# Optimization experiments

Hardware: AMD Instinct MI355X
Metric: run time of the kernel (lower is better)

The kernel has to match this reference:

```python
import jax, jax.numpy as jnp
import numpy as np

S, IN, H, D, B, BOT, IMG, TXT = 4, 4096, 2048, 6, 1024, 128, 768, 768


def _gelu(x):
    # torch nn.GELU default = exact erf gelu
    return jax.nn.gelu(x, approximate=False)


def _ln(x, g, b, eps=1e-5):
    mu = jnp.mean(x, axis=-1, keepdims=True)
    var = jnp.mean(jnp.square(x - mu), axis=-1, keepdims=True)
    return g * (x - mu) / jnp.sqrt(var + eps) + b


def setup_inputs() -> dict:
    key = jax.random.key(0)
    ks = jax.random.split(key, 16)
    n = lambda k, shp, s=0.02: jax.random.normal(k, shp, dtype=jnp.float32) * s
    return dict(
        voxels=jax.random.normal(ks[0], (B, IN), dtype=jnp.float32),
        subject_ids=jax.random.randint(ks[1], (B,), 0, S, dtype=jnp.int32),
        # per-subject encoder params, stacked on leading subject axis S
        ad_down_w=n(ks[2], (S, IN, BOT)), ad_down_b=n(ks[3], (S, BOT)),
        ad_up_w=n(ks[4], (S, BOT, IN)), ad_up_b=n(ks[5], (S, IN)),
        enc_w=n(ks[6], (S, IN, H)), enc_b=n(ks[7], (S, H)),
        enc_ln_g=jnp.ones((S, H), jnp.float32), enc_ln_b=jnp.zeros((S, H), jnp.float32),
        # shared ResidualStack params, stacked on leading depth axis D
        bb_w=n(ks[8], (D, H, H)), bb_b=n(ks[9], (D, H)),
        bb_ln_g=jnp.ones((D, H), jnp.float32), bb_ln_b=jnp.zeros((D, H), jnp.float32),
        # heads
        img_w=n(ks[10], (H, IMG)), img_b=n(ks[11], (IMG,)),
        txt_w=n(ks[12], (H, TXT)), txt_b=n(ks[13], (TXT,)),
    )


def _forward(voxels, subject_ids, ad_down_w, ad_down_b, ad_up_w, ad_up_b,
             enc_w, enc_b, enc_ln_g, enc_ln_b, bb_w, bb_b, bb_ln_g, bb_ln_b,
             img_w, img_b, txt_w, txt_b):
    # --- subject-routed encoders (dense dispatch over the small fixed subject set) ---
    def enc_one(dw, db, uw, ub, ew, eb, g, be):
        # BottleneckAdapter: x + up(gelu(down(x)))
        h = voxels + _gelu(voxels @ dw + db) @ uw + ub          # [B, IN]
        # Linear -> LayerNorm -> GELU (Dropout is identity in eval)
        return _gelu(_ln(h @ ew + eb, g, be))                    # [B, H]

    feats_all = jax.vmap(enc_one)(ad_down_w, ad_down_b, ad_up_w, ad_up_b,
                                  enc_w, enc_b, enc_ln_g, enc_ln_b)  # [S, B, H]
    x = feats_all[subject_ids, jnp.arange(voxels.shape[0])]          # [B, H] pick own subject

    # --- shared ResidualStack: x = x + gelu(ln(linear(x))) per block ---
    def step(x, p):
        w, b, g, be = p
        return x + _gelu(_ln(x @ w + b, g, be)), None

    x, _ = jax.lax.scan(step, x, (bb_w, bb_b, bb_ln_g, bb_ln_b))

    return x @ img_w + img_b, x @ txt_w + txt_b  # (image_embedding, text_embedding)


def reference(voxels, subject_ids, ad_down_w, ad_down_b, ad_up_w, ad_up_b,
              enc_w, enc_b, enc_ln_g, enc_ln_b, bb_w, bb_b, bb_ln_g, bb_ln_b,
              img_w, img_b, txt_w, txt_b):
    return _forward(voxels, subject_ids, ad_down_w, ad_down_b, ad_up_w, ad_up_b,
                    enc_w, enc_b, enc_ln_g, enc_ln_b, bb_w, bb_b, bb_ln_g, bb_ln_b,
                    img_w, img_b, txt_w, txt_b)
```

## Files before the change

kernel.cpp:

```cpp
#include <hip/hip_runtime.h>
#include <hip/hip_bf16.h>
#include <stdint.h>

typedef __bf16 bf16x8 __attribute__((ext_vector_type(8)));
typedef float  f32x4  __attribute__((ext_vector_type(4)));

#define DEV __device__ __forceinline__

constexpr int SUBJ  = 4;
constexpr int IN    = 4096;
constexpr int H     = 2048;
constexpr int DEPTH = 6;
constexpr int BATCH = 1024;
constexpr int BOT   = 128;
constexpr int IMG   = 768;
constexpr int TXT   = 768;
constexpr int MP    = 1408;
constexpr int MT    = 11;

DEV float gelu_exact(float x){ return 0.5f*x*(1.0f + erff(x*0.70710678118654752440f)); }

DEV uint32_t pk_bf16(float a, float b){
  __hip_bfloat16 ha = __float2bfloat16(a), hb = __float2bfloat16(b);
  return (uint32_t)*reinterpret_cast<uint16_t*>(&ha)
       | ((uint32_t)*reinterpret_cast<uint16_t*>(&hb) << 16);
}

__global__ void sort_kernel(const int* __restrict__ ids, int* __restrict__ rowmap,
                            int* __restrict__ tileS){
  __shared__ int hist[16][4];
  __shared__ int basew[16][4];
  __shared__ int pstart[5];
  int tid = threadIdx.x;
  if (tid < MP) rowmap[tid] = -1;
  if (tid + 1024 < MP) rowmap[tid + 1024] = -1;
  int w = tid >> 6, lane = tid & 63;
  int my = ids[tid];
  unsigned long long mymask = 0ull;
  #pragma unroll
  for (int s = 0; s < 4; ++s){
    unsigned long long m = __ballot(my == s);
    if (lane == 0) hist[w][s] = (int)__popcll(m);
    if (s == my) mymask = m;
  }
  int myrank = (int)__popcll(mymask & ((1ull << lane) - 1ull));
  __syncthreads();
  if (tid == 0){
    for (int s = 0; s < 4; ++s){
      int run = 0;
      for (int ww = 0; ww < 16; ++ww){ basew[ww][s] = run; run += hist[ww][s]; }
      hist[0][s] = run;
    }
    pstart[0] = 0;
    for (int s = 0; s < 4; ++s) pstart[s+1] = pstart[s] + ((hist[0][s] + 127) & ~127);
  }
  __syncthreads();
  int pos = pstart[my] + basew[w][my] + myrank;
  rowmap[pos] = tid;
  if (tid < MT){
    int row0 = tid << 7, s = -1;
    for (int ss = 0; ss < 4; ++ss) if (row0 >= pstart[ss] && row0 < pstart[ss+1]) s = ss;
    tileS[tid] = s;
  }
}

__global__ void gather_voxels(const float* __restrict__ vox, const int* __restrict__ rowmap,
                              __hip_bfloat16* __restrict__ Vs){
  int r = blockIdx.x, tid = threadIdx.x;
  int orig = rowmap[r];
  #pragma unroll
  for (int i = 0; i < 4; ++i){
    int c = (i*256 + tid) << 2;
    float4 v = {0.f,0.f,0.f,0.f};
    if (orig >= 0) v = *reinterpret_cast<const float4*>(vox + (size_t)orig*IN + c);
    __hip_bfloat16 o[4] = {__float2bfloat16(v.x), __float2bfloat16(v.y),
                           __float2bfloat16(v.z), __float2bfloat16(v.w)};
    *reinterpret_cast<uint2*>(Vs + (size_t)r*IN + c) = *reinterpret_cast<const uint2*>(o);
  }
}

enum { EPI_SPLIT = 0, EPI_RES_BF16 = 1, EPI_HEADS = 3 };

template<int EPI, int TAG>
__global__ __launch_bounds__(256, 2)
void gemm_bf16(const __hip_bfloat16* __restrict__ A, int lda,
               const float* __restrict__ Bw, int ldn, long long wsub,
               const int* __restrict__ tileS, const int* __restrict__ rowmap,
               int nx, int qnt, int ksplit,
               const float* __restrict__ bias, int biassub,
               const float* __restrict__ resid, int ldres,
               float* __restrict__ outf, __hip_bfloat16* __restrict__ outb, int ldo,
               size_t pstride, const float* __restrict__ Bw2)
{
  int b   = blockIdx.x;
  int xcd = b & 7;
  int r0  = b >> 3;
  int mt  = r0 % MT;
  int q   = r0 / MT;
  int kzi = xcd / nx + (q / qnt) * (8 / nx);
  int nt  = (q % qnt) * nx + (xcd % nx);

  int s = tileS[mt];
  if (s < 0) return;
  const __hip_bfloat16* Ab = A + (size_t)mt*128*lda;

  const float* Bb;
  int ntl = nt;
  if constexpr (EPI == EPI_HEADS){
    if (nt < 6){ Bb = Bw  + (size_t)nt*128; }
    else       { Bb = Bw2 + (size_t)(nt-6)*128; }
    ntl = nt;
  } else {
    Bb = Bw + (size_t)s*wsub + (size_t)nt*128;
  }

  int kb = kzi * ksplit;
  int nk = ksplit >> 6;

  __shared__ __hip_bfloat16 sA[2][128*64];
  __shared__ __hip_bfloat16 sB[2][128*64];

  int tid = threadIdx.x;
  int lane = tid & 63;
  int wv = tid >> 6, wr = wv >> 1, wc = wv & 1;

  int kq = tid >> 5;
  int nq = tid & 31;
  int n4 = nq << 2;

  f32x4 acc[4][4];
  #pragma unroll
  for (int i = 0; i < 4; ++i)
    #pragma unroll
    for (int j = 0; j < 4; ++j) acc[i][j] = (f32x4){0.f,0.f,0.f,0.f};

  auto stageA = [&](int buf, int k0){
    #pragma unroll
    for (int i = 0; i < 4; ++i){
      int cell = i*256 + tid;
      int row = cell >> 3, cc = cell & 7;
      int kg = k0 + ((cc ^ (row & 7)) << 3);
      __builtin_amdgcn_global_load_lds(
        (const __attribute__((address_space(1))) void*)(Ab + (size_t)row*lda + kg),
        (__attribute__((address_space(3))) void*)(&sA[buf][cell<<3]), 16, 0, 0);
    }
  };

  auto stageB_load = [&](int k0g, float4* F){
    const float* p = Bb + (size_t)(k0g + (kq<<3))*ldn + n4;
    #pragma unroll
    for (int rr = 0; rr < 8; ++rr)
      F[rr] = *reinterpret_cast<const float4*>(p + (size_t)rr*ldn);
  };
  auto stageB_write = [&](int buf, const float4* F){
    #pragma unroll
    for (int j = 0; j < 4; ++j){
      int n = n4 + j;
      int cell = (kq ^ (n >> 3) ^ n) & 7;
      uint4 d;
      d.x = pk_bf16(((const float*)&F[0])[j], ((const float*)&F[1])[j]);
      d.y = pk_bf16(((const float*)&F[2])[j], ((const float*)&F[3])[j]);
      d.z = pk_bf16(((const float*)&F[4])[j], ((const float*)&F[5])[j]);
      d.w = pk_bf16(((const float*)&F[6])[j], ((const float*)&F[7])[j]);
      *reinterpret_cast<uint4*>(&sB[buf][(n<<6) + (cell<<3)]) = d;
    }
  };

  float4 F[8];
  stageB_load(kb, F);
  stageA(0, kb);
  stageB_write(0, F);
  __syncthreads();

  for (int t = 0; t < nk; ++t){
    if (t+1 < nk){
      stageB_load(kb + ((t+1)<<6), F);
      stageA((t+1)&1, kb + ((t+1)<<6));
    }
    const char* baseA = (const char*)(&sA[t&1][0]);
    const char* baseB = (const char*)(&sB[t&1][0]);
    int rA = (wr<<6) + (lane & 15);
    int rB = (wc<<6) + (lane & 15);
    #pragma unroll
    for (int kk = 0; kk < 2; ++kk){
      int koffA = ((((kk<<5) + ((lane>>4)<<3)) << 1)) ^ ((lane & 7) << 4);
      bf16x8 av[4], bv[4];
      #pragma unroll
      for (int f = 0; f < 4; ++f){
        int rowA = rA + f*16;
        av[f] = *reinterpret_cast<const bf16x8*>(baseA + (size_t)rowA*128 + koffA);
        int rowB = rB + f*16;
        int cellB = (((kk<<2) + (lane>>4)) ^ (rowB >> 3) ^ rowB) & 7;
        bv[f] = *reinterpret_cast<const bf16x8*>(baseB + (size_t)rowB*128 + (cellB<<4));
      }
      #pragma unroll
      for (int i = 0; i < 4; ++i)
        #pragma unroll
        for (int j = 0; j < 4; ++j)
          acc[i][j] = __builtin_amdgcn_mfma_f32_16x16x32_bf16(av[i], bv[j], acc[i][j], 0, 0, 0);
    }
    if (t+1 < nk) stageB_write((t+1)&1, F);
    __syncthreads();
  }

  #pragma unroll
  for (int i = 0; i < 4; ++i){
    int rbase = (mt<<7) + (wr<<6) + (i<<4) + ((lane>>4)<<2);
    #pragma unroll
    for (int j = 0; j < 4; ++j){
      int colp = (wc<<6) + (j<<4) + (lane & 15);
      #pragma unroll
      for (int qq = 0; qq < 4; ++qq){
        int r = rbase + qq;
        float v = acc[i][j][qq];
        if constexpr (EPI == EPI_SPLIT){
          int col = (nt<<7) + colp;
          outf[(size_t)kzi*pstride + (size_t)r*ldo + col] = v;
        } else if constexpr (EPI == EPI_RES_BF16){
          int col = (nt<<7) + colp;
          int orig = rowmap[r];
          if (orig >= 0){
            v += bias[(size_t)s*biassub + col] + resid[(size_t)orig*ldres + col];
            outb[(size_t)r*ldo + col] = __float2bfloat16(v);
          }
        } else {
          int col = (ntl<<7) + colp;
          outf[(size_t)kzi*pstride + (size_t)r*ldo + col] = v;
        }
      }
    }
  }
}

__global__ void t1_epilogue(const float* __restrict__ Tp, const float* __restrict__ db,
                            const int* __restrict__ rowmap, const int* __restrict__ tileS,
                            __hip_bfloat16* __restrict__ T1){
  int idx = blockIdx.x*256 + threadIdx.x;
  int r = idx >> 7, c = idx & 127;
  float v = 0.f;
  if (rowmap[r] >= 0){
    int s = tileS[r >> 7];
    float acc = 0.f;
    #pragma unroll
    for (int p = 0; p < 32; ++p) acc += Tp[(size_t)p*MP*BOT + idx];
    v = gelu_exact(acc + db[s*BOT + c]);
  }
  T1[idx] = __float2bfloat16(v);
}

template<int RES, int NPART>
__global__ void ln_gelu_kernel(const float* __restrict__ Zp, size_t pstride,
                               const float* __restrict__ g,
                               const float* __restrict__ b, int gsub,
                               const float* __restrict__ lb,
                               const int* __restrict__ tileS, const int* __restrict__ rowmap,
                               float* __restrict__ Xf, __hip_bfloat16* __restrict__ Xb){
  int r = blockIdx.x, tid = threadIdx.x;
  size_t rowoff = (size_t)r * H;
  int c0 = tid << 3;
  int orig = rowmap[r];
  if (orig < 0){
    float4 zf = {0.f,0.f,0.f,0.f};
    *reinterpret_cast<float4*>(Xf + rowoff + c0)     = zf;
    *reinterpret_cast<float4*>(Xf + rowoff + c0 + 4) = zf;
    uint4 zu = {0u,0u,0u,0u};
    *reinterpret_cast<uint4*>(Xb + rowoff + c0) = zu;
    return;
  }
  int si = gsub ? tileS[r>>7] : 0;
  const float* gp  = g  + (size_t)si*gsub;
  const float* bp  = b  + (size_t)si*gsub;
  const float* lbp = lb + (size_t)si*gsub;
  float z[8];
  #pragma unroll
  for (int j = 0; j < 8; ++j) z[j] = lbp[c0+j];
  #pragma unroll
  for (int p = 0; p < NPART; ++p){
    float4 v1 = *reinterpret_cast<const float4*>(Zp + p*pstride + rowoff + c0);
    float4 v2 = *reinterpret_cast<const float4*>(Zp + p*pstride + rowoff + c0 + 4);
    z[0]+=v1.x; z[1]+=v1.y; z[2]+=v1.z; z[3]+=v1.w;
    z[4]+=v2.x; z[5]+=v2.y; z[6]+=v2.z; z[7]+=v2.w;
  }
  float s1 = 0.f, s2 = 0.f;
  #pragma unroll
  for (int j = 0; j < 8; ++j){ s1 += z[j]; s2 += z[j]*z[j]; }
  #pragma unroll
  for (int m = 32; m >= 1; m >>= 1){ s1 += __shfl_xor(s1, m); s2 += __shfl_xor(s2, m); }
  __shared__ float red[4][2];
  int wv = tid >> 6, lane = tid & 63;
  if (lane == 0){ red[wv][0] = s1; red[wv][1] = s2; }
  __syncthreads();
  s1 = red[0][0]+red[1][0]+red[2][0]+red[3][0];
  s2 = red[0][1]+red[1][1]+red[2][1]+red[3][1];
  const float invH = 1.f / (float)H;
  float mu  = s1 * invH;
  float var = s2 * invH - mu*mu;
  float rs  = rsqrtf(var + 1e-5f);
  float o[8];
  #pragma unroll
  for (int j = 0; j < 8; ++j){
    float t = (z[j]-mu)*rs*gp[c0+j] + bp[c0+j];
    o[j] = gelu_exact(t);
  }
  if constexpr (RES){
    float4 x1 = *reinterpret_cast<const float4*>(Xf + rowoff + c0);
    float4 x2 = *reinterpret_cast<const float4*>(Xf + rowoff + c0 + 4);
    o[0]+=x1.x; o[1]+=x1.y; o[2]+=x1.z; o[3]+=x1.w;
    o[4]+=x2.x; o[5]+=x2.y; o[6]+=x2.z; o[7]+=x2.w;
  }
  float4 w1 = {o[0],o[1],o[2],o[3]}, w2 = {o[4],o[5],o[6],o[7]};
  *reinterpret_cast<float4*>(Xf + rowoff + c0)     = w1;
  *reinterpret_cast<float4*>(Xf + rowoff + c0 + 4) = w2;
  __hip_bfloat16 ob[8];
  #pragma unroll
  for (int j = 0; j < 8; ++j) ob[j] = __float2bfloat16(o[j]);
  *reinterpret_cast<uint4*>(Xb + rowoff + c0) = *reinterpret_cast<const uint4*>(ob);
}

__global__ void head_combine(const float* __restrict__ Hp, size_t pstride,
                             const float* __restrict__ img_b, const float* __restrict__ txt_b,
                             const int* __restrict__ rowmap,
                             float* __restrict__ oimg, float* __restrict__ otxt){
  int r = blockIdx.x;
  int orig = rowmap[r];
  if (orig < 0) return;
  int col = threadIdx.x << 2;
  size_t base = (size_t)r*(IMG+TXT) + col;
  float4 v0 = *reinterpret_cast<const float4*>(Hp + base);
  float4 v1 = *reinterpret_cast<const float4*>(Hp + pstride + base);
  float4 bb = (col < IMG)
            ? *reinterpret_cast<const float4*>(img_b + col)
            : *reinterpret_cast<const float4*>(txt_b + (col - IMG));
  float4 o = {v0.x+v1.x+bb.x, v0.y+v1.y+bb.y, v0.z+v1.z+bb.z, v0.w+v1.w+bb.w};
  if (col < IMG) *reinterpret_cast<float4*>(oimg + (size_t)orig*IMG + col) = o;
  else           *reinterpret_cast<float4*>(otxt + (size_t)orig*TXT + (col-IMG)) = o;
}

extern "C" void kernel_launch(void* const* d_in, const int* in_sizes, int n_in,
                              void* d_out, int out_size, void* d_ws, size_t ws_size,
                              hipStream_t stream){
  (void)in_sizes; (void)n_in; (void)out_size; (void)ws_size;
  const float* vox       = (const float*)d_in[0];
  const int*   ids       = (const int*)  d_in[1];
  const float* ad_down_w = (const float*)d_in[2];
  const float* ad_down_b = (const float*)d_in[3];
  const float* ad_up_w   = (const float*)d_in[4];
  const float* ad_up_b   = (const float*)d_in[5];
  const float* enc_w     = (const float*)d_in[6];
  const float* enc_b     = (const float*)d_in[7];
  const float* enc_ln_g  = (const float*)d_in[8];
  const float* enc_ln_bb = (const float*)d_in[9];
  const float* bb_w      = (const float*)d_in[10];
  const float* bb_b      = (const float*)d_in[11];
  const float* bb_ln_g   = (const float*)d_in[12];
  const float* bb_ln_b   = (const float*)d_in[13];
  const float* img_w     = (const float*)d_in[14];
  const float* img_b     = (const float*)d_in[15];
  const float* txt_w     = (const float*)d_in[16];
  const float* txt_b     = (const float*)d_in[17];
  float* out = (float*)d_out;

  char* wp = (char*)d_ws;
  auto alloc = [&](size_t bytes)->char*{ char* p = wp; wp += (bytes + 255) & ~(size_t)255; return p; };
  int* rowmap = (int*)alloc(MP * sizeof(int));
  int* tileS  = (int*)alloc(MT * sizeof(int));
  __hip_bfloat16* Vs    = (__hip_bfloat16*)alloc((size_t)MP*IN*2);
  float* T1p            = (float*)alloc((size_t)32*MP*BOT*4);
  __hip_bfloat16* T1    = (__hip_bfloat16*)alloc((size_t)MP*BOT*2);
  __hip_bfloat16* Hs    = (__hip_bfloat16*)alloc((size_t)MP*IN*2);
  float* Zp             = (float*)alloc((size_t)8*MP*H*4);
  float* Hp             = (float*)alloc((size_t)2*MP*(IMG+TXT)*4);
  float* Xf             = (float*)alloc((size_t)MP*H*4);
  __hip_bfloat16* Xb    = (__hip_bfloat16*)alloc((size_t)MP*H*2);

  const size_t ZPS = (size_t)MP*H;
  const size_t TPS = (size_t)MP*BOT;
  const size_t HPS = (size_t)MP*(IMG+TXT);

  sort_kernel<<<1, 1024, 0, stream>>>(ids, rowmap, tileS);
  gather_voxels<<<MP, 256, 0, stream>>>(vox, rowmap, Vs);

  gemm_bf16<EPI_SPLIT,1><<<MT*32, 256, 0, stream>>>(
      Vs, IN, ad_down_w, BOT, (long long)IN*BOT, tileS, rowmap, 1, 1, 128,
      nullptr, 0, nullptr, 0, T1p, nullptr, BOT, TPS, nullptr);
  t1_epilogue<<<MP*BOT/256, 256, 0, stream>>>(T1p, ad_down_b, rowmap, tileS, T1);

  gemm_bf16<EPI_RES_BF16,2><<<MT*32, 256, 0, stream>>>(
      T1, BOT, ad_up_w, IN, (long long)BOT*IN, tileS, rowmap, 8, 4, 128,
      ad_up_b, IN, vox, IN, nullptr, Hs, IN, 0, nullptr);

  gemm_bf16<EPI_SPLIT,3><<<MT*16*8, 256, 0, stream>>>(
      Hs, IN, enc_w, H, (long long)IN*H, tileS, rowmap, 1, 16, 512,
      nullptr, 0, nullptr, 0, Zp, nullptr, H, ZPS, nullptr);
  ln_gelu_kernel<0,8><<<MP, 256, 0, stream>>>(Zp, ZPS, enc_ln_g, enc_ln_bb, H, enc_b,
                                              tileS, rowmap, Xf, Xb);

  for (int d = 0; d < DEPTH; ++d){
    gemm_bf16<EPI_SPLIT,4><<<MT*16*2, 256, 0, stream>>>(
        Xb, H, bb_w + (size_t)d*H*H, H, 0, tileS, rowmap, 4, 4, 1024,
        nullptr, 0, nullptr, 0, Zp, nullptr, H, ZPS, nullptr);
    ln_gelu_kernel<1,2><<<MP, 256, 0, stream>>>(Zp, ZPS, bb_ln_g + (size_t)d*H,
                                                bb_ln_b + (size_t)d*H, 0, bb_b + (size_t)d*H,
                                                tileS, rowmap, Xf, Xb);
  }

  gemm_bf16<EPI_HEADS,5><<<MT*12*2, 256, 0, stream>>>(
      Xb, H, img_w, IMG, 0, tileS, rowmap, 4, 3, 1024,
      nullptr, 0, nullptr, 0, Hp, nullptr, IMG+TXT, HPS, txt_w);
  head_combine<<<MP, 384, 0, stream>>>(Hp, HPS, img_b, txt_b, rowmap,
                                       out, out + (size_t)BATCH*IMG);
}
```

Baseline: 496.0 us.

## Pre-convert all weights to bf16 once per call and retune GEMM split-K

Adds a grid-stride kernel that converts every fp32 weight tensor into one contiguous bf16 workspace before the GEMMs. Each GEMM then loads bf16 weights directly, which halves the bytes it streams per K-step and removes the per-tile fp32-to-bf16 packing. It also retunes split-K factors for the down-projection and encoder GEMMs and shrinks the partial-sum buffers to match. The trade-off is a full extra read and write of every weight tensor on each call, about 400 MB of traffic.

```diff
diff --git a/kernel.cpp b/kernel.cpp
--- a/kernel.cpp
+++ b/kernel.cpp
@@ -20,10 +20,28 @@
 
 DEV float gelu_exact(float x){ return 0.5f*x*(1.0f + erff(x*0.70710678118654752440f)); }
 
-DEV uint32_t pk_bf16(float a, float b){
-  __hip_bfloat16 ha = __float2bfloat16(a), hb = __float2bfloat16(b);
-  return (uint32_t)*reinterpret_cast<uint16_t*>(&ha)
-       | ((uint32_t)*reinterpret_cast<uint16_t*>(&hb) << 16);
+DEV uint16_t bf16_bits(float x){
+  __hip_bfloat16 h = __float2bfloat16(x);
+  return *reinterpret_cast<uint16_t*>(&h);
+}
+
+struct CvtSeg { const float* src; size_t dst_off; };
+struct CvtParams { CvtSeg s[6]; size_t total_items; };
+
+__global__ void convert_weights(CvtParams p, __hip_bfloat16* __restrict__ dst){
+  size_t stride = (size_t)gridDim.x * blockDim.x;
+  for (size_t it = (size_t)blockIdx.x*blockDim.x + threadIdx.x; it < p.total_items; it += stride){
+    size_t e = it << 3;
+    int si = 0;
+    #pragma unroll
+    for (int i = 1; i < 6; ++i) if (e >= p.s[i].dst_off) si = i;
+    const float* s = p.s[si].src + (e - p.s[si].dst_off);
+    float4 a = *reinterpret_cast<const float4*>(s);
+    float4 b = *reinterpret_cast<const float4*>(s + 4);
+    uint16_t o[8] = {bf16_bits(a.x), bf16_bits(a.y), bf16_bits(a.z), bf16_bits(a.w),
+                     bf16_bits(b.x), bf16_bits(b.y), bf16_bits(b.z), bf16_bits(b.w)};
+    *reinterpret_cast<uint4*>(dst + e) = *reinterpret_cast<const uint4*>(o);
+  }
 }
 
 __global__ void sort_kernel(const int* __restrict__ ids, int* __restrict__ rowmap,
@@ -84,13 +102,13 @@
 template<int EPI, int TAG>
 __global__ __launch_bounds__(256, 2)
 void gemm_bf16(const __hip_bfloat16* __restrict__ A, int lda,
-               const float* __restrict__ Bw, int ldn, long long wsub,
+               const __hip_bfloat16* __restrict__ Bw, int ldn, long long wsub,
                const int* __restrict__ tileS, const int* __restrict__ rowmap,
                int nx, int qnt, int ksplit,
                const float* __restrict__ bias, int biassub,
                const float* __restrict__ resid, int ldres,
                float* __restrict__ outf, __hip_bfloat16* __restrict__ outb, int ldo,
-               size_t pstride, const float* __restrict__ Bw2)
+               size_t pstride, const __hip_bfloat16* __restrict__ Bw2)
 {
   int b   = blockIdx.x;
   int xcd = b & 7;
@@ -104,7 +122,7 @@
   if (s < 0) return;
   const __hip_bfloat16* Ab = A + (size_t)mt*128*lda;
 
-  const float* Bb;
+  const __hip_bfloat16* Bb;
   int ntl = nt;
   if constexpr (EPI == EPI_HEADS){
     if (nt < 6){ Bb = Bw  + (size_t)nt*128; }
@@ -146,27 +164,30 @@
     }
   };
 
-  auto stageB_load = [&](int k0g, float4* F){
-    const float* p = Bb + (size_t)(k0g + (kq<<3))*ldn + n4;
+  auto stageB_load = [&](int k0g, uint2* F){
+    const __hip_bfloat16* p = Bb + (size_t)(k0g + (kq<<3))*ldn + n4;
     #pragma unroll
     for (int rr = 0; rr < 8; ++rr)
-      F[rr] = *reinterpret_cast<const float4*>(p + (size_t)rr*ldn);
+      F[rr] = *reinterpret_cast<const uint2*>(p + (size_t)rr*ldn);
   };
-  auto stageB_write = [&](int buf, const float4* F){
+  auto stageB_write = [&](int buf, const uint2* F){
     #pragma unroll
     for (int j = 0; j < 4; ++j){
       int n = n4 + j;
       int cell = (kq ^ (n >> 3) ^ n) & 7;
+      auto US = [&](int rr)->uint32_t{
+        return (((const uint32_t*)&F[rr])[j >> 1] >> ((j & 1) * 16)) & 0xffffu;
+      };
       uint4 d;
-      d.x = pk_bf16(((const float*)&F[0])[j], ((const float*)&F[1])[j]);
-      d.y = pk_bf16(((const float*)&F[2])[j], ((const float*)&F[3])[j]);
-      d.z = pk_bf16(((const float*)&F[4])[j], ((const float*)&F[5])[j]);
-      d.w = pk_bf16(((const float*)&F[6])[j], ((const float*)&F[7])[j]);
+      d.x = US(0) | (US(1) << 16);
+      d.y = US(2) | (US(3) << 16);
+      d.z = US(4) | (US(5) << 16);
+      d.w = US(6) | (US(7) << 16);
       *reinterpret_cast<uint4*>(&sB[buf][(n<<6) + (cell<<3)]) = d;
     }
   };
 
-  float4 F[8];
+  uint2 F[8];
   stageB_load(kb, F);
   stageA(0, kb);
   stageB_write(0, F);
@@ -232,6 +253,7 @@
   }
 }
 
+template<int NPART>
 __global__ void t1_epilogue(const float* __restrict__ Tp, const float* __restrict__ db,
                             const int* __restrict__ rowmap, const int* __restrict__ tileS,
                             __hip_bfloat16* __restrict__ T1){
@@ -242,7 +264,7 @@
     int s = tileS[r >> 7];
     float acc = 0.f;
     #pragma unroll
-    for (int p = 0; p < 32; ++p) acc += Tp[(size_t)p*MP*BOT + idx];
+    for (int p = 0; p < NPART; ++p) acc += Tp[(size_t)p*MP*BOT + idx];
     v = gelu_exact(acc + db[s*BOT + c]);
   }
   T1[idx] = __float2bfloat16(v);
@@ -360,16 +382,30 @@
   const float* txt_b     = (const float*)d_in[17];
   float* out = (float*)d_out;
 
+  const size_t N_DOWN = (size_t)SUBJ*IN*BOT;
+  const size_t N_UP   = (size_t)SUBJ*BOT*IN;
+  const size_t N_ENC  = (size_t)SUBJ*IN*H;
+  const size_t N_BB   = (size_t)DEPTH*H*H;
+  const size_t N_IMG  = (size_t)H*IMG;
+  const size_t N_TXT  = (size_t)H*TXT;
+
   char* wp = (char*)d_ws;
   auto alloc = [&](size_t bytes)->char*{ char* p = wp; wp += (bytes + 255) & ~(size_t)255; return p; };
   int* rowmap = (int*)alloc(MP * sizeof(int));
   int* tileS  = (int*)alloc(MT * sizeof(int));
+  __hip_bfloat16* Wbf = (__hip_bfloat16*)alloc((N_DOWN+N_UP+N_ENC+N_BB+N_IMG+N_TXT)*2);
+  __hip_bfloat16* w_down = Wbf;
+  __hip_bfloat16* w_up   = w_down + N_DOWN;
+  __hip_bfloat16* w_enc  = w_up   + N_UP;
+  __hip_bfloat16* w_bb   = w_enc  + N_ENC;
+  __hip_bfloat16* w_img  = w_bb   + N_BB;
+  __hip_bfloat16* w_txt  = w_img  + N_IMG;
   __hip_bfloat16* Vs    = (__hip_bfloat16*)alloc((size_t)MP*IN*2);
-  float* T1p            = (float*)alloc((size_t)32*MP*BOT*4);
+  float* T1p            = (float*)alloc((size_t)16*MP*BOT*4);
   __hip_bfloat16* T1    = (__hip_bfloat16*)alloc((size_t)MP*BOT*2);
   __hip_bfloat16* Hs    = (__hip_bfloat16*)alloc((size_t)MP*IN*2);
-  float* Zp             = (float*)alloc((size_t)8*MP*H*4);
-  float* Hp             = (float*)alloc((size_t)2*MP*(IMG+TXT)*4);
+  float* Zp             = (float*)alloc((size_t)4*MP*H*4);
+  float* Hp             = Zp;
   float* Xf             = (float*)alloc((size_t)MP*H*4);
   __hip_bfloat16* Xb    = (__hip_bfloat16*)alloc((size_t)MP*H*2);
 
@@ -377,36 +413,47 @@
   const size_t TPS = (size_t)MP*BOT;
   const size_t HPS = (size_t)MP*(IMG+TXT);
 
+  CvtParams cp;
+  size_t off = 0;
+  cp.s[0] = {ad_down_w, off}; off += N_DOWN;
+  cp.s[1] = {ad_up_w,   off}; off += N_UP;
+  cp.s[2] = {enc_w,     off}; off += N_ENC;
+  cp.s[3] = {bb_w,      off}; off += N_BB;
+  cp.s[4] = {img_w,     off}; off += N_IMG;
+  cp.s[5] = {txt_w,     off}; off += N_TXT;
+  cp.total_items = off >> 3;
+  convert_weights<<<2048, 256, 0, stream>>>(cp, Wbf);
+
   sort_kernel<<<1, 1024, 0, stream>>>(ids, rowmap, tileS);
   gather_voxels<<<MP, 256, 0, stream>>>(vox, rowmap, Vs);
 
-  gemm_bf16<EPI_SPLIT,1><<<MT*32, 256, 0, stream>>>(
-      Vs, IN, ad_down_w, BOT, (long long)IN*BOT, tileS, rowmap, 1, 1, 128,
+  gemm_bf16<EPI_SPLIT,1><<<MT*16, 256, 0, stream>>>(
+      Vs, IN, w_down, BOT, (long long)IN*BOT, tileS, rowmap, 1, 1, 256,
       nullptr, 0, nullptr, 0, T1p, nullptr, BOT, TPS, nullptr);
-  t1_epilogue<<<MP*BOT/256, 256, 0, stream>>>(T1p, ad_down_b, rowmap, tileS, T1);
+  t1_epilogue<16><<<MP*BOT/256, 256, 0, stream>>>(T1p, ad_down_b, rowmap, tileS, T1);
 
   gemm_bf16<EPI_RES_BF16,2><<<MT*32, 256, 0, stream>>>(
-      T1, BOT, ad_up_w, IN, (long long)BOT*IN, tileS, rowmap, 8, 4, 128,
+      T1, BOT, w_up, IN, (long long)BOT*IN, tileS, rowmap, 8, 4, 128,
       ad_up_b, IN, vox, IN, nullptr, Hs, IN, 0, nullptr);
 
-  gemm_bf16<EPI_SPLIT,3><<<MT*16*8, 256, 0, stream>>>(
-      Hs, IN, enc_w, H, (long long)IN*H, tileS, rowmap, 1, 16, 512,
+  gemm_bf16<EPI_SPLIT,3><<<MT*8*8, 256, 0, stream>>>(
+      Hs, IN, w_enc, H, (long long)IN*H, tileS, rowmap, 2, 8, 1024,
       nullptr, 0, nullptr, 0, Zp, nullptr, H, ZPS, nullptr);
-  ln_gelu_kernel<0,8><<<MP, 256, 0, stream>>>(Zp, ZPS, enc_ln_g, enc_ln_bb, H, enc_b,
+  ln_gelu_kernel<0,4><<<MP, 256, 0, stream>>>(Zp, ZPS, enc_ln_g, enc_ln_bb, H, enc_b,
                                               tileS, rowmap, Xf, Xb);
 
   for (int d = 0; d < DEPTH; ++d){
-    gemm_bf16<EPI_SPLIT,4><<<MT*16*2, 256, 0, stream>>>(
-        Xb, H, bb_w + (size_t)d*H*H, H, 0, tileS, rowmap, 4, 4, 1024,
+    gemm_bf16<EPI_SPLIT,4><<<MT*4*8, 256, 0, stream>>>(
+        Xb, H, w_bb + (size_t)d*H*H, H, 0, tileS, rowmap, 4, 4, 1024,
         nullptr, 0, nullptr, 0, Zp, nullptr, H, ZPS, nullptr);
     ln_gelu_kernel<1,2><<<MP, 256, 0, stream>>>(Zp, ZPS, bb_ln_g + (size_t)d*H,
                                                 bb_ln_b + (size_t)d*H, 0, bb_b + (size_t)d*H,
                                                 tileS, rowmap, Xf, Xb);
   }
 
-  gemm_bf16<EPI_HEADS,5><<<MT*12*2, 256, 0, stream>>>(
-      Xb, H, img_w, IMG, 0, tileS, rowmap, 4, 3, 1024,
-      nullptr, 0, nullptr, 0, Hp, nullptr, IMG+TXT, HPS, txt_w);
+  gemm_bf16<EPI_HEADS,5><<<MT*3*8, 256, 0, stream>>>(
+      Xb, H, w_img, IMG, 0, tileS, rowmap, 4, 3, 1024,
+      nullptr, 0, nullptr, 0, Hp, nullptr, IMG+TXT, HPS, w_txt);
   head_combine<<<MP, 384, 0, stream>>>(Hp, HPS, img_b, txt_b, rowmap,
                                        out, out + (size_t)BATCH*IMG);
 }
```

Measured after the change: 470.9 us. 1.05x faster.
